# Optimization experiments

Hardware: AMD Instinct MI355X
Metric: run time of the kernel (lower is better)

Reference implementation:

```python
import jax, jax.numpy as jnp
import numpy as np

HIDDEN = 1024
INTER = 4096

def setup_inputs() -> dict:
    key = jax.random.key(0)
    k1, k2, k3, k4, k5 = jax.random.split(key, 5)
    hidden_states = jax.random.normal(k1, (4, 2048, HIDDEN), dtype=jnp.float32)
    # Linear params: W stored pre-transposed as [in, out], matching W = dense.weight.t()
    W1 = jax.random.normal(k2, (HIDDEN, INTER), dtype=jnp.float32) * (1.0 / np.sqrt(HIDDEN))
    b1 = jax.random.normal(k3, (INTER,), dtype=jnp.float32) * 0.02
    W2 = jax.random.normal(k4, (INTER, HIDDEN), dtype=jnp.float32) * (1.0 / np.sqrt(INTER))
    b2 = jax.random.normal(k5, (HIDDEN,), dtype=jnp.float32) * 0.02
    return {"hidden_states": hidden_states, "W1": W1, "b1": b1, "W2": W2, "b2": b2}

def reference(hidden_states, W1, b1, W2, b2):
    # Tiled loops in the original are exactly a dense 2-layer MLP with ReLU.
    h = jax.nn.relu(jnp.einsum('bsh,hi->bsi', hidden_states, W1) + b1)
    return jnp.einsum('bsi,ih->bsh', h, W2) + b2
```

## Files before the change

kernel.cpp:

```cpp
#include <hip/hip_runtime.h>
#include <cstddef>

typedef short short8 __attribute__((ext_vector_type(8)));
typedef unsigned short ushort8 __attribute__((ext_vector_type(8)));
typedef float f32x4 __attribute__((ext_vector_type(4)));

#define AS1(p) ((const __attribute__((address_space(1))) void*)(p))
#define AS3(p) ((__attribute__((address_space(3))) void*)(p))

__device__ __forceinline__ unsigned short f2bf(float f) {
  unsigned int u = __builtin_bit_cast(unsigned int, f);
  u += 0x7FFFu + ((u >> 16) & 1u);
  return (unsigned short)(u >> 16);
}

__device__ __forceinline__ void gload_lds16(const void* g, void* l) {
  __builtin_amdgcn_global_load_lds(AS1(g), AS3(l), 16, 0, 0);
}

template <int N>
__device__ __forceinline__ void vwait() {
  asm volatile("s_waitcnt vmcnt(%0)" :: "n"(N) : "memory");
}

__global__ __launch_bounds__(256)
void prep_fused(const float* __restrict__ X,
                const float* __restrict__ W1,
                const float* __restrict__ W2,
                unsigned short* __restrict__ Xbf,
                unsigned short* __restrict__ W1t,
                unsigned short* __restrict__ W2t) {
  const int b   = blockIdx.x;
  const int tid = threadIdx.x;

  if (b >= 8192) {
    const size_t i = (size_t)(b - 8192) * 256 + tid;
    float4 v = *reinterpret_cast<const float4*>(X + i * 4);
    ushort4 o;
    o.x = f2bf(v.x); o.y = f2bf(v.y); o.z = f2bf(v.z); o.w = f2bf(v.w);
    *reinterpret_cast<ushort4*>(Xbf + i * 4) = o;
    return;
  }

  __shared__ float tile[32][33];
  const float* in;
  unsigned short* out;
  int Kd, Nd, n0, k0;
  if (b < 4096) {
    in = W1; out = W1t; Kd = 1024; Nd = 4096;
    n0 = (b & 127) * 32;
    k0 = (b >> 7) * 32;
  } else {
    const int b2 = b - 4096;
    in = W2; out = W2t; Kd = 4096; Nd = 1024;
    n0 = (b2 & 31) * 32;
    k0 = (b2 >> 5) * 32;
  }
  const int tx = tid & 31;
  const int ty = tid >> 5;
#pragma unroll
  for (int i = 0; i < 4; ++i)
    tile[ty + i * 8][tx] = in[(size_t)(k0 + ty + i * 8) * Nd + n0 + tx];
  __syncthreads();
#pragma unroll
  for (int i = 0; i < 4; ++i)
    out[(size_t)(n0 + ty + i * 8) * Kd + k0 + tx] = f2bf(tile[tx][ty + i * 8]);
}

__global__ void cvt_f32_bf16(const float* __restrict__ in,
                             unsigned short* __restrict__ out, int n4) {
  int i = blockIdx.x * blockDim.x + threadIdx.x;
  if (i >= n4) return;
  float4 v = *reinterpret_cast<const float4*>(in + (size_t)i * 4);
  ushort4 o;
  o.x = f2bf(v.x); o.y = f2bf(v.y); o.z = f2bf(v.z); o.w = f2bf(v.w);
  *reinterpret_cast<ushort4*>(out + (size_t)i * 4) = o;
}

__global__ void transpose_cvt(const float* __restrict__ in,
                              unsigned short* __restrict__ out,
                              int Kd, int Nd) {
  __shared__ float tile[32][33];
  const int n0 = blockIdx.x * 32;
  const int k0 = blockIdx.y * 32;
  const int tx = threadIdx.x;
  const int ty = threadIdx.y;
#pragma unroll
  for (int i = 0; i < 4; ++i)
    tile[ty + i * 8][tx] = in[(size_t)(k0 + ty + i * 8) * Nd + n0 + tx];
  __syncthreads();
#pragma unroll
  for (int i = 0; i < 4; ++i)
    out[(size_t)(n0 + ty + i * 8) * Kd + k0 + tx] = f2bf(tile[tx][ty + i * 8]);
}

template <int BN, int RELU_BF16_OUT>
__global__ __launch_bounds__(512, 2)
void gemm_cf(const unsigned short* __restrict__ A, int lda,
             const unsigned short* __restrict__ B, int ldb,
             const float* __restrict__ bias,
             void* __restrict__ C, int ldc, int K, int nbx) {
  constexpr int PWN    = BN / 4;
  constexpr int NB     = PWN / 16;
  constexpr int AUNITS = 4;
  constexpr int BUNITS = BN / 64;
  constexpr int LPT    = AUNITS + BUNITS;
  constexpr int BUFSZ  = 32768 + BN * 128;
  extern __shared__ char lds[];

  const int tid  = threadIdx.x;
  const int lane = tid & 63;
  const int wid  = tid >> 6;
  const int wm   = wid >> 2;
  const int wn   = wid & 3;

  const int cpx     = gridDim.x >> 3;
  const int logical = (blockIdx.x & 7) * cpx + (blockIdx.x >> 3);
  const int m0 = (logical / nbx) * 256;
  const int n0 = (logical % nbx) * BN;

  f32x4 acc[8][NB];
#pragma unroll
  for (int i = 0; i < 8; ++i)
#pragma unroll
    for (int j = 0; j < NB; ++j)
      acc[i][j] = (f32x4){0.f, 0.f, 0.f, 0.f};

  size_t aofs[AUNITS], bofs[BUNITS];
  const int ldst = (tid & 448) * 16;
#pragma unroll
  for (int u = 0; u < AUNITS; ++u) {
    const int s   = (u * 512 + tid) * 16;
    const int nat = s ^ (((s >> 7) & 7) << 4);
    aofs[u] = (size_t)(m0 + (nat >> 7)) * lda + ((nat & 127) >> 1);
  }
#pragma unroll
  for (int u = 0; u < BUNITS; ++u) {
    const int s   = (u * 512 + tid) * 16;
    const int nat = s ^ (((s >> 7) & 7) << 4);
    bofs[u] = (size_t)(n0 + (nat >> 7)) * ldb + ((nat & 127) >> 1);
  }

  auto stage = [&](int d, int k0) {
    char* ab = lds + d * BUFSZ;
    char* bb = ab + 32768;
#pragma unroll
    for (int u = 0; u < AUNITS; ++u)
      gload_lds16(A + aofs[u] + k0, ab + u * 8192 + ldst);
#pragma unroll
    for (int u = 0; u < BUNITS; ++u)
      gload_lds16(B + bofs[u] + k0, bb + u * 8192 + ldst);
  };

  int ard[8][2], brd[NB][2];
#pragma unroll
  for (int mi = 0; mi < 8; ++mi)
#pragma unroll
    for (int kk = 0; kk < 2; ++kk) {
      const int nat = (wm * 128 + mi * 16 + (lane & 15)) * 128 +
                      kk * 64 + (lane >> 4) * 16;
      ard[mi][kk] = nat ^ (((nat >> 7) & 7) << 4);
    }
#pragma unroll
  for (int ni = 0; ni < NB; ++ni)
#pragma unroll
    for (int kk = 0; kk < 2; ++kk) {
      const int nat = (wn * PWN + ni * 16 + (lane & 15)) * 128 +
                      kk * 64 + (lane >> 4) * 16;
      brd[ni][kk] = 32768 + (nat ^ (((nat >> 7) & 7) << 4));
    }

  stage(0, 0);

  const int NT = K >> 6;
  for (int t = 0; t < NT; ++t) {
    const int cur = t & 1;
    if (t + 1 < NT) {
      stage(cur ^ 1, (t + 1) << 6);
      vwait<LPT>();
    } else {
      vwait<0>();
    }
    __builtin_amdgcn_s_barrier();

    char* ab = lds + cur * BUFSZ;
#pragma unroll
    for (int kk = 0; kk < 2; ++kk) {
      short8 bfv[NB];
#pragma unroll
      for (int ni = 0; ni < NB; ++ni)
        bfv[ni] = *reinterpret_cast<const short8*>(ab + brd[ni][kk]);
#pragma unroll
      for (int mi = 0; mi < 8; ++mi) {
        const short8 af = *reinterpret_cast<const short8*>(ab + ard[mi][kk]);
#pragma unroll
        for (int ni = 0; ni < NB; ++ni)
          acc[mi][ni] = __builtin_amdgcn_mfma_f32_16x16x32_bf16(
              af, bfv[ni], acc[mi][ni], 0, 0, 0);
      }
    }
    __builtin_amdgcn_s_barrier();
  }

  const int row0 = m0 + wm * 128 + (lane >> 4) * 4;
  const int col0 = n0 + wn * PWN + (lane & 15);
#pragma unroll
  for (int ni = 0; ni < NB; ++ni) {
    const int c = col0 + ni * 16;
    const float bv = bias[c];
#pragma unroll
    for (int mi = 0; mi < 8; ++mi) {
#pragma unroll
      for (int r = 0; r < 4; ++r) {
        const size_t idx = (size_t)(row0 + mi * 16 + r) * ldc + c;
        float v = acc[mi][ni][r] + bv;
        if (RELU_BF16_OUT) {
          v = v > 0.f ? v : 0.f;
          ((unsigned short*)C)[idx] = f2bf(v);
        } else {
          ((float*)C)[idx] = v;
        }
      }
    }
  }
}

template <int A_F32, int RELU_BF16_OUT>
__global__ __launch_bounds__(256, 2)
void gemm_bf16(const void* __restrict__ Ap, int lda,
               const unsigned short* __restrict__ B, int ldb,
               const float* __restrict__ bias,
               void* __restrict__ C, int ldc,
               int K, int beta) {
  __shared__ char lds[32768];
  char* const As = lds;
  char* const Bs = lds + 16384;

  const int tid  = threadIdx.x;
  const int lane = tid & 63;
  const int w    = tid >> 6;
  const int wm   = w >> 1;
  const int wn   = w & 1;
  const int m0   = blockIdx.y * 128;
  const int n0   = blockIdx.x * 128;

  f32x4 acc[4][4];
#pragma unroll
  for (int i = 0; i < 4; ++i)
#pragma unroll
    for (int j = 0; j < 4; ++j)
      acc[i][j] = (f32x4){0.f, 0.f, 0.f, 0.f};

  int srow[4], scol[4], sbase[4];
#pragma unroll
  for (int j = 0; j < 4; ++j) {
    const int stored  = (j * 256 + tid) * 16;
    const int natural = stored ^ (((stored >> 7) & 7) << 4);
    srow[j]  = natural >> 7;
    scol[j]  = (natural & 127) >> 1;
    sbase[j] = (j * 256 + (tid & 192)) * 16;
  }

  size_t agofs[4];
  int ast[4];
  if (A_F32) {
#pragma unroll
    for (int pq = 0; pq < 4; ++pq) {
      const int idx = pq * 256 + tid;
      const int rr  = idx >> 3;
      const int kbe = (idx & 7) * 8;
      agofs[pq] = (size_t)(m0 + rr) * lda + kbe;
      const int nat = rr * 128 + kbe * 2;
      ast[pq] = nat ^ (((nat >> 7) & 7) << 4);
    }
  }

  const int nsteps = K >> 6;
  for (int ks = 0; ks < nsteps; ++ks) {
    const int k0 = ks << 6;
    if (A_F32) {
      const float* Af = (const float*)Ap;
#pragma unroll
      for (int pq = 0; pq < 4; ++pq) {
        const float* sp = Af + agofs[pq] + k0;
        float4 x0 = *reinterpret_cast<const float4*>(sp);
        float4 x1 = *reinterpret_cast<const float4*>(sp + 4);
        ushort8 v;
        v[0] = f2bf(x0.x); v[1] = f2bf(x0.y); v[2] = f2bf(x0.z); v[3] = f2bf(x0.w);
        v[4] = f2bf(x1.x); v[5] = f2bf(x1.y); v[6] = f2bf(x1.z); v[7] = f2bf(x1.w);
        *reinterpret_cast<ushort8*>(As + ast[pq]) = v;
      }
    } else {
      const unsigned short* Ab = (const unsigned short*)Ap;
#pragma unroll
      for (int j = 0; j < 4; ++j)
        gload_lds16(Ab + (size_t)(m0 + srow[j]) * lda + (k0 + scol[j]),
                    As + sbase[j]);
    }
#pragma unroll
    for (int j = 0; j < 4; ++j)
      gload_lds16(B + (size_t)(n0 + srow[j]) * ldb + (k0 + scol[j]),
                  Bs + sbase[j]);
    __syncthreads();

#pragma unroll
    for (int kk = 0; kk < 2; ++kk) {
      const int kb = kk * 64 + (lane >> 4) * 16;
      short8 af[4], bfv[4];
#pragma unroll
      for (int mi = 0; mi < 4; ++mi) {
        int nat = (wm * 64 + mi * 16 + (lane & 15)) * 128 + kb;
        int st  = nat ^ (((nat >> 7) & 7) << 4);
        af[mi] = *reinterpret_cast<const short8*>(As + st);
      }
#pragma unroll
      for (int ni = 0; ni < 4; ++ni) {
        int nat = (wn * 64 + ni * 16 + (lane & 15)) * 128 + kb;
        int st  = nat ^ (((nat >> 7) & 7) << 4);
        bfv[ni] = *reinterpret_cast<const short8*>(Bs + st);
      }
#pragma unroll
      for (int mi = 0; mi < 4; ++mi)
#pragma unroll
        for (int ni = 0; ni < 4; ++ni)
          acc[mi][ni] = __builtin_amdgcn_mfma_f32_16x16x32_bf16(
              af[mi], bfv[ni], acc[mi][ni], 0, 0, 0);
    }
    __syncthreads();
  }

  const int row0 = m0 + wm * 64 + (lane >> 4) * 4;
  const int col0 = n0 + wn * 64 + (lane & 15);
#pragma unroll
  for (int ni = 0; ni < 4; ++ni) {
    const int c = col0 + ni * 16;
    const float bv = beta ? 0.f : bias[c];
#pragma unroll
    for (int mi = 0; mi < 4; ++mi) {
#pragma unroll
      for (int rr = 0; rr < 4; ++rr) {
        const size_t idx = (size_t)(row0 + mi * 16 + rr) * ldc + c;
        float v = acc[mi][ni][rr] + bv;
        if (RELU_BF16_OUT) {
          v = v > 0.f ? v : 0.f;
          ((unsigned short*)C)[idx] = f2bf(v);
        } else {
          if (beta) v += ((float*)C)[idx];
          ((float*)C)[idx] = v;
        }
      }
    }
  }
}

extern "C" void kernel_launch(void* const* d_in, const int* in_sizes, int n_in,
                              void* d_out, int out_size, void* d_ws, size_t ws_size,
                              hipStream_t stream) {
  const float* X  = (const float*)d_in[0];
  const float* W1 = (const float*)d_in[1];
  const float* b1 = (const float*)d_in[2];
  const float* W2 = (const float*)d_in[3];
  const float* b2 = (const float*)d_in[4];
  float* out = (float*)d_out;

  const int M = 8192, H = 1024, I = 4096;
  const size_t MB = 1024 * 1024;

  char* ws = (char*)d_ws;
  unsigned short* W1t = (unsigned short*)ws;
  unsigned short* W2t = (unsigned short*)(ws + 8 * MB);

  if (ws_size >= 80 * MB) {
    unsigned short* Xbf = (unsigned short*)((char*)d_out + 16 * MB);
    unsigned short* Hbf = (unsigned short*)(ws + 16 * MB);
    prep_fused<<<16384, 256, 0, stream>>>(X, W1, W2, Xbf, W1t, W2t);
    gemm_cf<256, 1><<<512, 512, 131072, stream>>>(
        Xbf, H, W1t, H, b1, Hbf, I, H, I / 256);
    gemm_cf<128, 0><<<256, 512, 98304, stream>>>(
        Hbf, I, W2t, I, b2, out, H, I, H / 128);
    return;
  }

  transpose_cvt<<<dim3(I / 32, H / 32), dim3(32, 8), 0, stream>>>(W1, W1t, H, I);
  transpose_cvt<<<dim3(H / 32, I / 32), dim3(32, 8), 0, stream>>>(W2, W2t, I, H);

  int Ic, useXbf;
  unsigned short* Xbf = nullptr;
  unsigned short* Hc;
  if (ws_size >= 64 * MB) {
    Ic = 2048; useXbf = 1;
    Xbf = (unsigned short*)(ws + 16 * MB);
    Hc  = (unsigned short*)(ws + 32 * MB);
  } else if (ws_size >= 48 * MB) {
    Ic = 1024; useXbf = 1;
    Xbf = (unsigned short*)(ws + 16 * MB);
    Hc  = (unsigned short*)(ws + 32 * MB);
  } else if (ws_size >= 32 * MB) {
    Ic = 1024; useXbf = 0;
    Hc  = (unsigned short*)(ws + 16 * MB);
  } else if (ws_size >= 24 * MB) {
    Ic = 512;  useXbf = 0;
    Hc  = (unsigned short*)(ws + 16 * MB);
  } else if (ws_size >= 20 * MB) {
    Ic = 256;  useXbf = 0;
    Hc  = (unsigned short*)(ws + 16 * MB);
  } else {
    Ic = 128;  useXbf = 0;
    Hc  = (unsigned short*)(ws + 16 * MB);
  }

  if (useXbf) {
    int n4 = (M * H) / 4;
    cvt_f32_bf16<<<(n4 + 255) / 256, 256, 0, stream>>>(X, Xbf, n4);
  }

  const int nch = I / Ic;
  for (int c = 0; c < nch; ++c) {
    const int i0 = c * Ic;
    if (useXbf)
      gemm_bf16<0, 1><<<dim3(Ic / 128, M / 128), 256, 0, stream>>>(
          Xbf, H, W1t + (size_t)i0 * H, H, b1 + i0, Hc, Ic, H, 0);
    else
      gemm_bf16<1, 1><<<dim3(Ic / 128, M / 128), 256, 0, stream>>>(
          X, H, W1t + (size_t)i0 * H, H, b1 + i0, Hc, Ic, H, 0);
    gemm_bf16<0, 0><<<dim3(H / 128, M / 128), 256, 0, stream>>>(
        Hc, Ic, W2t + i0, I, b2, out, H, Ic, c > 0);
  }
}
```

Measured before the change: 165.8 us.

## Restructure GEMM into four-quadrant pipelined phases with LDS-staged coalesced epilogue

Measured after the change: 157.2 us, median of 3. -5.2%, faster.

```diff
diff --git a/kernel.cpp b/kernel.cpp
--- a/kernel.cpp
+++ b/kernel.cpp
@@ -94,132 +94,188 @@
     out[(size_t)(n0 + ty + i * 8) * Kd + k0 + tx] = f2bf(tile[tx][ty + i * 8]);
 }
 
+#define QPH(D, QM, QN, RDA, RDB, STAGE, WAITC)                                 \
+  {                                                                            \
+    if (RDA) {                                                                 \
+      char* ab = lds + (D) * 32768 + (QM) * 16384;                             \
+      _Pragma("unroll")                                                        \
+      for (int mi = 0; mi < 4; ++mi)                                           \
+        _Pragma("unroll")                                                      \
+        for (int kk = 0; kk < 2; ++kk)                                         \
+          aF[mi][kk] = *reinterpret_cast<const short8*>(ab + ardA[mi][kk]);    \
+    }                                                                          \
+    if (RDB) {                                                                 \
+      char* bb = lds + 65536 + (D) * 2 * BHB + (QN) * BHB;                     \
+      _Pragma("unroll")                                                        \
+      for (int ni = 0; ni < NF; ++ni)                                          \
+        _Pragma("unroll")                                                      \
+        for (int kk = 0; kk < 2; ++kk)                                         \
+          bF[QN][ni][kk] = *reinterpret_cast<const short8*>(bb + brdB[ni][kk]);\
+    }                                                                          \
+    STAGE;                                                                     \
+    __builtin_amdgcn_s_setprio(1);                                             \
+    _Pragma("unroll")                                                          \
+    for (int mi = 0; mi < 4; ++mi)                                             \
+      _Pragma("unroll")                                                        \
+      for (int ni = 0; ni < NF; ++ni)                                          \
+        _Pragma("unroll")                                                      \
+        for (int kk = 0; kk < 2; ++kk)                                         \
+          acc[QM][QN][mi][ni] = __builtin_amdgcn_mfma_f32_16x16x32_bf16(       \
+              aF[mi][kk], bF[QN][ni][kk], acc[QM][QN][mi][ni], 0, 0, 0);       \
+    __builtin_amdgcn_s_setprio(0);                                             \
+    WAITC;                                                                     \
+    __builtin_amdgcn_s_barrier();                                              \
+  }
+
 template <int BN, int RELU_BF16_OUT>
 __global__ __launch_bounds__(512, 2)
-void gemm_cf(const unsigned short* __restrict__ A, int lda,
-             const unsigned short* __restrict__ B, int ldb,
-             const float* __restrict__ bias,
-             void* __restrict__ C, int ldc, int K, int nbx) {
-  constexpr int PWN    = BN / 4;
-  constexpr int NB     = PWN / 16;
-  constexpr int AUNITS = 4;
-  constexpr int BUNITS = BN / 64;
-  constexpr int LPT    = AUNITS + BUNITS;
-  constexpr int BUFSZ  = 32768 + BN * 128;
+void gemm_q(const unsigned short* __restrict__ A, int lda,
+            const unsigned short* __restrict__ B, int ldb,
+            const float* __restrict__ bias,
+            void* __restrict__ C, int ldc, int K, int nbx) {
+  constexpr int NF  = BN / 128;
+  constexpr int LA  = 2;
+  constexpr int LB  = BN / 128;
+  constexpr int BHB = BN * 64;
   extern __shared__ char lds[];
 
   const int tid  = threadIdx.x;
   const int lane = tid & 63;
   const int wid  = tid >> 6;
-  const int wm   = wid >> 2;
-  const int wn   = wid & 3;
+  const int wm2  = wid >> 2;
+  const int wn4  = wid & 3;
 
   const int cpx     = gridDim.x >> 3;
   const int logical = (blockIdx.x & 7) * cpx + (blockIdx.x >> 3);
   const int m0 = (logical / nbx) * 256;
   const int n0 = (logical % nbx) * BN;
 
-  f32x4 acc[8][NB];
-#pragma unroll
-  for (int i = 0; i < 8; ++i)
-#pragma unroll
-    for (int j = 0; j < NB; ++j)
-      acc[i][j] = (f32x4){0.f, 0.f, 0.f, 0.f};
-
-  size_t aofs[AUNITS], bofs[BUNITS];
-  const int ldst = (tid & 448) * 16;
-#pragma unroll
-  for (int u = 0; u < AUNITS; ++u) {
+  f32x4 acc[2][2][4][NF];
+#pragma unroll
+  for (int a = 0; a < 2; ++a)
+#pragma unroll
+    for (int b = 0; b < 2; ++b)
+#pragma unroll
+      for (int c = 0; c < 4; ++c)
+#pragma unroll
+        for (int d = 0; d < NF; ++d)
+          acc[a][b][c][d] = (f32x4){0.f, 0.f, 0.f, 0.f};
+
+  size_t aG[2], bG[2];
+#pragma unroll
+  for (int u = 0; u < 2; ++u) {
     const int s   = (u * 512 + tid) * 16;
     const int nat = s ^ (((s >> 7) & 7) << 4);
-    aofs[u] = (size_t)(m0 + (nat >> 7)) * lda + ((nat & 127) >> 1);
-  }
-#pragma unroll
-  for (int u = 0; u < BUNITS; ++u) {
-    const int s   = (u * 512 + tid) * 16;
-    const int nat = s ^ (((s >> 7) & 7) << 4);
-    bofs[u] = (size_t)(n0 + (nat >> 7)) * ldb + ((nat & 127) >> 1);
-  }
-
-  auto stage = [&](int d, int k0) {
-    char* ab = lds + d * BUFSZ;
-    char* bb = ab + 32768;
-#pragma unroll
-    for (int u = 0; u < AUNITS; ++u)
-      gload_lds16(A + aofs[u] + k0, ab + u * 8192 + ldst);
-#pragma unroll
-    for (int u = 0; u < BUNITS; ++u)
-      gload_lds16(B + bofs[u] + k0, bb + u * 8192 + ldst);
+    aG[u] = (size_t)(m0 + (nat >> 7)) * lda + ((nat & 127) >> 1);
+    if (u < LB)
+      bG[u] = (size_t)(n0 + (nat >> 7)) * ldb + ((nat & 127) >> 1);
+    else
+      bG[u] = 0;
+  }
+  const int wb0 = (tid & 448) * 16;
+  const int wb1 = 8192 + wb0;
+
+  auto stageA = [&](int d, int h, int kel) {
+    char* dst = lds + d * 32768 + h * 16384;
+    gload_lds16(A + aG[0] + (size_t)h * 128 * lda + kel, dst + wb0);
+    gload_lds16(A + aG[1] + (size_t)h * 128 * lda + kel, dst + wb1);
   };
-
-  int ard[8][2], brd[NB][2];
-#pragma unroll
-  for (int mi = 0; mi < 8; ++mi)
+  auto stageB = [&](int d, int h, int kel) {
+    char* dst = lds + 65536 + d * 2 * BHB + h * BHB;
+    gload_lds16(B + bG[0] + (size_t)h * (BN / 2) * ldb + kel, dst + wb0);
+    if constexpr (LB == 2)
+      gload_lds16(B + bG[1] + (size_t)h * (BN / 2) * ldb + kel, dst + wb1);
+  };
+
+  int ardA[4][2], brdB[NF][2];
+#pragma unroll
+  for (int mi = 0; mi < 4; ++mi)
 #pragma unroll
     for (int kk = 0; kk < 2; ++kk) {
-      const int nat = (wm * 128 + mi * 16 + (lane & 15)) * 128 +
+      const int nat = (wm2 * 64 + mi * 16 + (lane & 15)) * 128 +
                       kk * 64 + (lane >> 4) * 16;
-      ard[mi][kk] = nat ^ (((nat >> 7) & 7) << 4);
-    }
-#pragma unroll
-  for (int ni = 0; ni < NB; ++ni)
+      ardA[mi][kk] = nat ^ (((nat >> 7) & 7) << 4);
+    }
+#pragma unroll
+  for (int ni = 0; ni < NF; ++ni)
 #pragma unroll
     for (int kk = 0; kk < 2; ++kk) {
-      const int nat = (wn * PWN + ni * 16 + (lane & 15)) * 128 +
+      const int nat = (wn4 * (BN / 8) + ni * 16 + (lane & 15)) * 128 +
                       kk * 64 + (lane >> 4) * 16;
-      brd[ni][kk] = 32768 + (nat ^ (((nat >> 7) & 7) << 4));
-    }
-
-  stage(0, 0);
-
+      brdB[ni][kk] = nat ^ (((nat >> 7) & 7) << 4);
+    }
+
+  stageA(0, 0, 0);
+  stageB(0, 0, 0);
+  stageB(0, 1, 0);
+  stageA(0, 1, 0);
+  vwait<LA + LB>();
+  __builtin_amdgcn_s_barrier();
+
+  short8 aF[4][2];
+  short8 bF[2][NF][2];
   const int NT = K >> 6;
-  for (int t = 0; t < NT; ++t) {
-    const int cur = t & 1;
-    if (t + 1 < NT) {
-      stage(cur ^ 1, (t + 1) << 6);
-      vwait<LPT>();
-    } else {
-      vwait<0>();
-    }
-    __builtin_amdgcn_s_barrier();
-
-    char* ab = lds + cur * BUFSZ;
-#pragma unroll
-    for (int kk = 0; kk < 2; ++kk) {
-      short8 bfv[NB];
-#pragma unroll
-      for (int ni = 0; ni < NB; ++ni)
-        bfv[ni] = *reinterpret_cast<const short8*>(ab + brd[ni][kk]);
-#pragma unroll
-      for (int mi = 0; mi < 8; ++mi) {
-        const short8 af = *reinterpret_cast<const short8*>(ab + ard[mi][kk]);
-#pragma unroll
-        for (int ni = 0; ni < NB; ++ni)
-          acc[mi][ni] = __builtin_amdgcn_mfma_f32_16x16x32_bf16(
-              af, bfv[ni], acc[mi][ni], 0, 0, 0);
-      }
-    }
-    __builtin_amdgcn_s_barrier();
-  }
-
-  const int row0 = m0 + wm * 128 + (lane >> 4) * 4;
-  const int col0 = n0 + wn * PWN + (lane & 15);
-#pragma unroll
-  for (int ni = 0; ni < NB; ++ni) {
-    const int c = col0 + ni * 16;
-    const float bv = bias[c];
-#pragma unroll
-    for (int mi = 0; mi < 8; ++mi) {
-#pragma unroll
-      for (int r = 0; r < 4; ++r) {
-        const size_t idx = (size_t)(row0 + mi * 16 + r) * ldc + c;
-        float v = acc[mi][ni][r] + bv;
-        if (RELU_BF16_OUT) {
-          v = v > 0.f ? v : 0.f;
-          ((unsigned short*)C)[idx] = f2bf(v);
-        } else {
-          ((float*)C)[idx] = v;
+  for (int it = 0; it < NT - 1; ++it) {
+    const int d = it & 1, e = d ^ 1;
+    const int nk = (it + 1) << 6;
+    QPH(d, 0, 0, 1, 1, stageA(e, 0, nk), vwait<2 * LA>());
+    QPH(d, 0, 1, 0, 1, stageB(e, 0, nk), (vwait<LA + LB>()));
+    QPH(d, 1, 0, 1, 0, stageB(e, 1, nk), vwait<2 * LB>());
+    QPH(d, 1, 1, 0, 0, stageA(e, 1, nk), (vwait<LB + LA>()));
+  }
+  {
+    const int d = (NT - 1) & 1;
+    QPH(d, 0, 0, 1, 1, ((void)0), vwait<LA>());
+    QPH(d, 0, 1, 0, 1, ((void)0), vwait<0>());
+    QPH(d, 1, 0, 1, 0, ((void)0), ((void)0));
+    QPH(d, 1, 1, 0, 0, ((void)0), ((void)0));
+  }
+
+  __syncthreads();
+  {
+#pragma unroll
+    for (int qm = 0; qm < 2; ++qm) {
+#pragma unroll
+      for (int qn = 0; qn < 2; ++qn) {
+#pragma unroll
+        for (int ni = 0; ni < NF; ++ni) {
+          const int c = qn * (BN / 2) + wn4 * (BN / 8) + ni * 16 + (lane & 15);
+          const float bv = bias[n0 + c];
+#pragma unroll
+          for (int mi = 0; mi < 4; ++mi) {
+#pragma unroll
+            for (int rr = 0; rr < 4; ++rr) {
+              const int row = qm * 128 + wm2 * 64 + mi * 16 +
+                              (lane >> 4) * 4 + rr;
+              float v = acc[qm][qn][mi][ni][rr] + bv;
+              if (RELU_BF16_OUT) {
+                v = v > 0.f ? v : 0.f;
+                const int byte = (row * 512 + c * 2) ^ ((row & 7) << 4);
+                *reinterpret_cast<unsigned short*>(lds + byte) = f2bf(v);
+              } else {
+                const int byte = (row * 512 + c * 4) ^ ((row & 7) << 4);
+                *reinterpret_cast<float*>(lds + byte) = v;
+              }
+            }
+          }
         }
+      }
+    }
+    __syncthreads();
+#pragma unroll
+    for (int i = 0; i < 16; ++i) {
+      const int idx  = i * 512 + tid;
+      const int row  = idx >> 5;
+      const int g    = idx & 31;
+      const int byte = (row * 512 + g * 16) ^ ((row & 7) << 4);
+      const uint4 val = *reinterpret_cast<const uint4*>(lds + byte);
+      if (RELU_BF16_OUT) {
+        unsigned short* dst = (unsigned short*)C +
+            (size_t)(m0 + row) * ldc + n0 + g * 8;
+        *reinterpret_cast<uint4*>(dst) = val;
+      } else {
+        float* dst = (float*)C + (size_t)(m0 + row) * ldc + n0 + g * 4;
+        *reinterpret_cast<uint4*>(dst) = val;
       }
     }
   }
@@ -374,9 +430,9 @@
     unsigned short* Xbf = (unsigned short*)((char*)d_out + 16 * MB);
     unsigned short* Hbf = (unsigned short*)(ws + 16 * MB);
     prep_fused<<<16384, 256, 0, stream>>>(X, W1, W2, Xbf, W1t, W2t);
-    gemm_cf<256, 1><<<512, 512, 131072, stream>>>(
+    gemm_q<256, 1><<<512, 512, 131072, stream>>>(
         Xbf, H, W1t, H, b1, Hbf, I, H, I / 256);
-    gemm_cf<128, 0><<<256, 512, 98304, stream>>>(
+    gemm_q<128, 0><<<256, 512, 131072, stream>>>(
         Hbf, I, W2t, I, b2, out, H, I, H / 128);
     return;
   }
```
